# Kernel tuning notes

Measured on AMD Instinct MI355X. Metric: run time of the kernel, lower is better.

Reference implementation:

```python
import jax, jax.numpy as jnp
import numpy as np

T, B, OBS, H, A = 128, 256, 128, 512, 18
LSTM_IN = H + A + 1  # trunk_out + one_hot(a) + r


def setup_inputs() -> dict:
    key = jax.random.key(0)
    ks = jax.random.split(key, 24)

    def rn(k, shape, scale=0.05):
        return jax.random.normal(k, shape, dtype=jnp.float32) * scale

    inp = {
        "o": jax.random.normal(ks[0], (T, B, OBS), dtype=jnp.float32),
        "a": jax.random.randint(ks[1], (T, B), 0, A, dtype=jnp.int32),
        "r": jax.random.normal(ks[2], (T, B), dtype=jnp.float32),
        "done": (jax.random.uniform(ks[3], (T, B)) < 0.05).astype(jnp.float32),
        "h0": jax.random.normal(ks[4], (B, H), dtype=jnp.float32) * 0.1,
        "c0": jax.random.normal(ks[5], (B, H), dtype=jnp.float32) * 0.1,
        # trunk
        "tW0": rn(ks[6], (OBS, H)), "tb0": jnp.zeros((H,), jnp.float32),
        "tW1": rn(ks[7], (H, H)), "tb1": jnp.zeros((H,), jnp.float32),
        # LSTM (PyTorch layout: gates stacked as [i, f, g, o])
        "W_ih": rn(ks[8], (4 * H, LSTM_IN)), "W_hh": rn(ks[9], (4 * H, H)),
        "b_ih": jnp.zeros((4 * H,), jnp.float32), "b_hh": jnp.zeros((4 * H,), jnp.float32),
        # advantage head
        "aW0": rn(ks[10], (H, H)), "ab0": jnp.zeros((H,), jnp.float32),
        "aW1": rn(ks[11], (H, A)), "ab1": jnp.zeros((A,), jnp.float32),
        # value head
        "vW0": rn(ks[12], (H, H)), "vb0": jnp.zeros((H,), jnp.float32),
        "vW1": rn(ks[13], (H, 1)), "vb1": jnp.zeros((1,), jnp.float32),
    }
    return inp


def _forward(o, a, r, done, h0, c0, tW0, tb0, tW1, tb1,
             W_ih, W_hh, b_ih, b_hh, aW0, ab0, aW1, ab1, vW0, vb0, vW1, vb1):
    # shared trunk: two Linear+ReLU layers, vectorized over T*B
    hidden = jax.nn.relu(jnp.einsum('tbi,ih->tbh', o, tW0) + tb0)
    hidden = jax.nn.relu(jnp.einsum('tbi,ih->tbh', hidden, tW1) + tb1)
    a_oh = jax.nn.one_hot(a, A, dtype=jnp.float32)          # [T,B,A]
    x = jnp.concatenate([hidden, r[..., None], a_oh], -1)    # [T,B,LSTM_IN]

    # precompute input projection for all steps (not state-dependent)
    xg = jnp.einsum('tbi,gi->tbg', x, W_ih) + b_ih + b_hh    # [T,B,4H]

    def step(carry, inp):
        h, c = carry
        xg_t, d_t = inp
        keep = (1.0 - d_t)[:, None]                          # per-step done reset
        h, c = h * keep, c * keep
        gates = xg_t + h @ W_hh.T                            # [B,4H]
        i, f, g, og = jnp.split(gates, 4, axis=-1)
        c = jax.nn.sigmoid(f) * c + jax.nn.sigmoid(i) * jnp.tanh(g)
        h = jax.nn.sigmoid(og) * jnp.tanh(c)
        return (h, c), h

    (hT, cT), hs = jax.lax.scan(step, (h0, c0), (xg, done))  # hs: [T,B,H]

    ah = jax.nn.relu(jnp.einsum('tbh,hk->tbk', hs, aW0) + ab0)
    adv = jnp.einsum('tbk,ka->tba', ah, aW1) + ab1            # [T,B,A]
    vh = jax.nn.relu(jnp.einsum('tbh,hk->tbk', hs, vW0) + vb0)
    val = jnp.einsum('tbk,kv->tbv', vh, vW1) + vb1            # [T,B,1]
    q = val + (adv - adv.mean(axis=-1, keepdims=True))
    return q, hT, cT


def reference(o, a, r, done, h0, c0, tW0, tb0, tW1, tb1,
              W_ih, W_hh, b_ih, b_hh, aW0, ab0, aW1, ab1, vW0, vb0, vW1, vb1):
    return _forward(o, a, r, done, h0, c0, tW0, tb0, tW1, tb1,
                    W_ih, W_hh, b_ih, b_hh, aW0, ab0, aW1, ab1, vW0, vb0, vW1, vb1)
```

## Files before the change

### kernel.cpp

```cpp
#include <hip/hip_runtime.h>
#include <cstdint>

typedef unsigned short u16;
typedef unsigned int u32;
typedef unsigned long long u64;
typedef float f32x4 __attribute__((ext_vector_type(4)));
typedef short s16x8 __attribute__((ext_vector_type(8)));

#define DEV static __device__ __forceinline__

#define TT 128
#define BB 256
#define OBSD 128
#define HHD 512
#define AD 18
#define GGD 2048
#define MMD 32768

DEV u16 f2bf(float f) {
  u32 u = __builtin_bit_cast(u32, f);
  u += 0x7fffu + ((u >> 16) & 1u);
  return (u16)(u >> 16);
}
DEV float bf2f(u16 h) { return __builtin_bit_cast(float, ((u32)h) << 16); }

DEV f32x4 mfma16x16x32(s16x8 a, s16x8 b, f32x4 c) {
  asm("v_mfma_f32_16x16x32_bf16 %0, %1, %2, %0" : "+v"(c) : "v"(a), "v"(b));
  return c;
}
DEV void fence_mfma_read(f32x4& x) { asm volatile("s_nop 7" : "+v"(x)); }
DEV void fence_mfma_srcc(f32x4& x) { asm volatile("s_nop 1" : "+v"(x)); }

typedef __attribute__((address_space(3))) char lds_char;
typedef __attribute__((address_space(1))) const char gl_char;
DEV void gload16(const char* g, char* l) {
  __builtin_amdgcn_global_load_lds((const gl_char*)g, (lds_char*)l, 16, 0, 0);
}

DEV float sigm(float x) { return 1.f / (1.f + __expf(-x)); }
DEV float tanh_fast(float x) {
  float t = __expf(-2.f * fabsf(x));
  float r = (1.f - t) / (1.f + t);
  return copysignf(r, x);
}

constexpr size_t OFF_FLAGS = 0;
constexpr size_t OFF_HRING = 524288;
constexpr size_t OFF_TW0T  = 1048576;
constexpr size_t OFF_TW1T  = 1179648;
constexpr size_t OFF_AW0T  = 1703936;
constexpr size_t OFF_VW0T  = 2228224;
constexpr size_t OFF_AW1T  = 2752512;
constexpr size_t OFF_VW1T  = 2770944;
constexpr size_t OFF_WIH   = 2772992;
constexpr size_t OFF_WHH   = 4870144;
constexpr size_t OFF_BSUM  = 6967296;
constexpr size_t OFF_WRC   = 6975488;
constexpr size_t OFF_WEMB  = 6983680;
constexpr size_t OFF_BCAT  = 7131136;
constexpr size_t OFF_OBF   = 8388608;
constexpr size_t OFF_BUF1  = 16777216;
constexpr size_t OFF_BUF2  = 50331648;
constexpr size_t OFF_BUF3  = 83886080;

__global__ __launch_bounds__(256) void prep(
    const float* __restrict__ o, const float* __restrict__ tW0,
    const float* __restrict__ tW1, const float* __restrict__ aW0,
    const float* __restrict__ vW0, const float* __restrict__ aW1,
    const float* __restrict__ vW1, const float* __restrict__ Wih,
    const float* __restrict__ WhhF, const float* __restrict__ bih,
    const float* __restrict__ bhh, const float* __restrict__ h0,
    const float* __restrict__ done, const float* __restrict__ ab0,
    const float* __restrict__ vb0,
    u16* __restrict__ o_bf, u16* __restrict__ tW0T, u16* __restrict__ tW1T,
    u16* __restrict__ aW0T, u16* __restrict__ vW0T, u16* __restrict__ aW1T,
    u16* __restrict__ vW1T, u16* __restrict__ WihB, u16* __restrict__ WhhB,
    float* __restrict__ bsum, float* __restrict__ wrc, float* __restrict__ wemb,
    float* __restrict__ bcat, u16* __restrict__ hring)
{
  const int total = 4178432;
  for (int id = blockIdx.x * 256 + threadIdx.x; id < total; id += gridDim.x * 256) {
    int i = id;
    if (i < 1048576) {
      float4 v = ((const float4*)o)[i];
      u16* dst = o_bf + (size_t)i * 4;
      dst[0] = f2bf(v.x); dst[1] = f2bf(v.y); dst[2] = f2bf(v.z); dst[3] = f2bf(v.w);
      continue;
    }
    i -= 1048576;
    if (i < 65536)  { int n = i >> 7, k = i & 127; tW0T[i] = f2bf(tW0[k * 512 + n]); continue; }
    i -= 65536;
    if (i < 262144) { int n = i >> 9, k = i & 511; tW1T[i] = f2bf(tW1[k * 512 + n]); continue; }
    i -= 262144;
    if (i < 262144) { int n = i >> 9, k = i & 511; aW0T[i] = f2bf(aW0[k * 512 + n]); continue; }
    i -= 262144;
    if (i < 262144) { int n = i >> 9, k = i & 511; vW0T[i] = f2bf(vW0[k * 512 + n]); continue; }
    i -= 262144;
    if (i < 9216)   { int n = i >> 9, k = i & 511; aW1T[i] = f2bf(aW1[k * 18 + n]); continue; }
    i -= 9216;
    if (i < 512)    { vW1T[i] = f2bf(vW1[i]); continue; }
    i -= 512;
    if (i < 1048576){ int g = i >> 9, k = i & 511; WihB[i] = f2bf(Wih[g * 531 + k]); continue; }
    i -= 1048576;
    if (i < 1048576){ WhhB[i] = f2bf(WhhF[i]); continue; }
    i -= 1048576;
    if (i < 2048)   { bsum[i] = bih[i] + bhh[i]; wrc[i] = Wih[i * 531 + 512]; continue; }
    i -= 2048;
    if (i < 36864)  { int j = i >> 11, g = i & 2047; wemb[i] = Wih[g * 531 + 513 + j]; continue; }
    i -= 36864;
    if (i < 1024)   { bcat[i] = (i < 512) ? ab0[i] : vb0[i - 512]; continue; }
    i -= 1024;
    { int b = i >> 9; hring[i] = f2bf(h0[i] * (1.f - done[b])); }
  }
}

template<int MODE>
__global__ __launch_bounds__(256) void gemm_bt(
    const u16* __restrict__ A, const u16* __restrict__ Bt, u16* __restrict__ C,
    int Mdim, int Ndim, int Kdim,
    const float* __restrict__ bias,
    const float* __restrict__ wrc, const float* __restrict__ wemb,
    const float* __restrict__ rin, const int* __restrict__ ain)
{
  __shared__ __align__(16) char smem[32768];
  const int tid = threadIdx.x;
  const int nTn = Ndim >> 7;
  int wg = blockIdx.x;
  {
    const int per = gridDim.x >> 3;
    wg = (wg & 7) * per + (wg >> 3);
  }
  const int tm = wg / nTn, tn = wg % nTn;
  const int wid = tid >> 6, lane = tid & 63;
  const int wr = wid >> 1, wc = wid & 1;
  const int l15 = lane & 15, l4 = lane >> 4;

  f32x4 acc[4][4];
#pragma unroll
  for (int i = 0; i < 4; ++i)
#pragma unroll
    for (int j = 0; j < 4; ++j) acc[i][j] = f32x4{0.f, 0.f, 0.f, 0.f};

  const int srow = lane >> 3;
  const int scolb = ((lane & 7) * 16) ^ (srow << 4);
  const size_t kd2 = (size_t)Kdim * 2;
  const char* Abase = (const char*)(A + (size_t)tm * 128 * Kdim);
  const char* Bbase = (const char*)(Bt + (size_t)tn * 128 * Kdim);
  const char* ga[4]; const char* gb[4]; char* la[4]; char* lb[4];
#pragma unroll
  for (int j = 0; j < 4; ++j) {
    const int row = wid * 32 + j * 8 + srow;
    ga[j] = Abase + (size_t)row * kd2 + scolb;
    gb[j] = Bbase + (size_t)row * kd2 + scolb;
    la[j] = smem + wid * 4096 + j * 1024;
    lb[j] = smem + 16384 + wid * 4096 + j * 1024;
  }

  for (int k0 = 0; k0 < Kdim; k0 += 64) {
    const size_t kb = (size_t)k0 * 2;
#pragma unroll
    for (int j = 0; j < 4; ++j) {
      gload16(ga[j] + kb, la[j]);
      gload16(gb[j] + kb, lb[j]);
    }
    __syncthreads();
#pragma unroll
    for (int kk = 0; kk < 2; ++kk) {
      s16x8 af[4], bfr[4];
#pragma unroll
      for (int i = 0; i < 4; ++i) {
        int ar = wr * 64 + i * 16 + l15;
        af[i] = *(const s16x8*)(smem + ((ar * 128 + kk * 64 + l4 * 16) ^ ((ar & 7) << 4)));
        int br = wc * 64 + i * 16 + l15;
        bfr[i] = *(const s16x8*)(smem + 16384 + ((br * 128 + kk * 64 + l4 * 16) ^ ((br & 7) << 4)));
      }
#pragma unroll
      for (int i = 0; i < 4; ++i)
#pragma unroll
        for (int j = 0; j < 4; ++j)
          acc[i][j] = mfma16x16x32(af[i], bfr[j], acc[i][j]);
    }
    __syncthreads();
  }

#pragma unroll
  for (int i = 0; i < 4; ++i)
#pragma unroll
    for (int j = 0; j < 4; ++j) fence_mfma_read(acc[i][j]);

#pragma unroll
  for (int i = 0; i < 4; ++i) {
    const int rowb = tm * 128 + wr * 64 + i * 16 + l4 * 4;
    float rv[4]; int av[4];
    if (MODE == 1) {
#pragma unroll
      for (int r = 0; r < 4; ++r) { rv[r] = rin[rowb + r]; av[r] = ain[rowb + r]; }
    }
#pragma unroll
    for (int j = 0; j < 4; ++j) {
      const int col = tn * 128 + wc * 64 + j * 16 + l15;
      const float bs = bias[col];
      if (MODE == 0) {
#pragma unroll
        for (int r = 0; r < 4; ++r) {
          float x = acc[i][j][r] + bs;
          x = fmaxf(x, 0.f);
          C[(size_t)(rowb + r) * Ndim + col] = f2bf(x);
        }
      } else {
        const float wcv = wrc[col];
#pragma unroll
        for (int r = 0; r < 4; ++r) {
          float x = acc[i][j][r] + bs + rv[r] * wcv + wemb[av[r] * GGD + col];
          C[(size_t)(rowb + r) * Ndim + col] = f2bf(x);
        }
      }
    }
  }
}

__global__ __launch_bounds__(256) void lstm_seq(
    const u16* __restrict__ xg, const u16* __restrict__ WhhB,
    const float* __restrict__ done, const float* __restrict__ c0,
    u16* __restrict__ hring, u16* __restrict__ hs,
    float* __restrict__ hT, float* __restrict__ cT, u32* __restrict__ flags)
{
  __shared__ __align__(16) char wsm[65536];
  const int tid = threadIdx.x;
  const int bg = blockIdx.x & 3;
  const int ug = blockIdx.x >> 2;
  const int b0 = bg * 64;
  const int u0 = ug * 16;

#pragma unroll
  for (int i = 0; i < 16; ++i) {
    int idx = i * 256 + tid;
    int lr = idx >> 6, c8 = idx & 63;
    int g = lr >> 4, uu = lr & 15;
    uint4 v = *(const uint4*)(WhhB + (size_t)(g * 512 + u0 + uu) * 512 + c8 * 8);
    *(uint4*)(wsm + ((lr * 1024 + c8 * 16) ^ ((lr & 7) << 4))) = v;
  }
  __syncthreads();

  const int wid = tid >> 6, lane = tid & 63;
  const int l15 = lane & 15, l4 = lane >> 4;
  const int mrow = wid * 16 + l4 * 4;
  const int afrow = b0 + wid * 16 + l15;
  const int u = u0 + l15;

  float creg[4], kc[4], kn[4];
#pragma unroll
  for (int r = 0; r < 4; ++r) {
    creg[r] = c0[(size_t)(b0 + mrow + r) * HHD + u];
    kc[r] = 1.f - done[b0 + mrow + r];
    kn[r] = 1.f - done[BB + b0 + mrow + r];
  }

  u16 xpf[16];
#pragma unroll
  for (int g = 0; g < 4; ++g)
#pragma unroll
    for (int r = 0; r < 4; ++r)
      xpf[g * 4 + r] = xg[(size_t)(b0 + mrow + r) * GGD + g * HHD + u];

  for (int t = 0; t < TT; ++t) {
    const u16* hsrc = hring + (size_t)(t & 1) * (BB * HHD);
    u16* hdst = hring + (size_t)((t + 1) & 1) * (BB * HHD);

    f32x4 acc[4];
#pragma unroll
    for (int g = 0; g < 4; ++g)
#pragma unroll
      for (int r = 0; r < 4; ++r)
        acc[g][r] = bf2f(xpf[g * 4 + r]);
#pragma unroll
    for (int g = 0; g < 4; ++g) fence_mfma_srcc(acc[g]);

    u64 aflo[16], afhi[16];
    const u64* hb = (const u64*)(hsrc + (size_t)afrow * HHD);
#pragma unroll
    for (int kk = 0; kk < 16; ++kk) {
      aflo[kk] = __hip_atomic_load(hb + kk * 8 + l4 * 2,
                                   __ATOMIC_RELAXED, __HIP_MEMORY_SCOPE_AGENT);
      afhi[kk] = __hip_atomic_load(hb + kk * 8 + l4 * 2 + 1,
                                   __ATOMIC_RELAXED, __HIP_MEMORY_SCOPE_AGENT);
    }
#pragma unroll
    for (int kk = 0; kk < 16; ++kk) {
      union { u64 q[2]; s16x8 v; } tmp;
      tmp.q[0] = aflo[kk]; tmp.q[1] = afhi[kk];
      s16x8 a = tmp.v;
#pragma unroll
      for (int g = 0; g < 4; ++g) {
        int br = g * 16 + l15;
        s16x8 b = *(const s16x8*)(wsm + ((br * 1024 + kk * 64 + l4 * 16) ^ ((br & 7) << 4)));
        acc[g] = mfma16x16x32(a, b, acc[g]);
      }
    }
#pragma unroll
    for (int g = 0; g < 4; ++g) fence_mfma_read(acc[g]);

    float hv_[4], cv_[4];
#pragma unroll
    for (int r = 0; r < 4; ++r) {
      float iv = sigm(acc[0][r]);
      float fv = sigm(acc[1][r]);
      float gv = tanh_fast(acc[2][r]);
      float ov = sigm(acc[3][r]);
      float c = fv * (creg[r] * kc[r]) + iv * gv;
      float h = ov * tanh_fast(c);
      creg[r] = c; cv_[r] = c; hv_[r] = h;
    }

    if (t < TT - 1) {
      u32 pw[4];
#pragma unroll
      for (int r = 0; r < 4; ++r) {
        u16 ob = f2bf(hv_[r] * kn[r]);
        u16 pb = (u16)__shfl_xor((int)ob, 1, 64);
        pw[r] = ((l15 & 1) == 0) ? ((u32)ob | ((u32)pb << 16))
                                 : ((u32)pb | ((u32)ob << 16));
      }
      {
        const int rb = (l15 & 1) * 2;
        u32* hd32 = (u32*)hdst;
        const int col2 = (u0 + (l15 & ~1)) >> 1;
        __hip_atomic_store(&hd32[(size_t)(b0 + mrow + rb) * 256 + col2], pw[rb],
                           __ATOMIC_RELAXED, __HIP_MEMORY_SCOPE_AGENT);
        __hip_atomic_store(&hd32[(size_t)(b0 + mrow + rb + 1) * 256 + col2], pw[rb + 1],
                           __ATOMIC_RELAXED, __HIP_MEMORY_SCOPE_AGENT);
      }
      __syncthreads();
      if (tid == 0)
        __hip_atomic_store(&flags[(bg * TT + t) * 32 + ug], 1u,
                           __ATOMIC_RELAXED, __HIP_MEMORY_SCOPE_AGENT);
#pragma unroll
      for (int r = 0; r < 4; ++r)
        hs[((size_t)t * BB + b0 + mrow + r) * HHD + u] = f2bf(hv_[r]);
#pragma unroll
      for (int g = 0; g < 4; ++g)
#pragma unroll
        for (int r = 0; r < 4; ++r)
          xpf[g * 4 + r] = xg[((size_t)(t + 1) * BB + b0 + mrow + r) * GGD + g * HHD + u];
#pragma unroll
      for (int r = 0; r < 4; ++r) {
        kc[r] = kn[r];
        kn[r] = (t + 2 < TT) ? (1.f - done[(size_t)(t + 2) * BB + b0 + mrow + r]) : 1.f;
      }
      if (tid < 32) {
        while (__hip_atomic_load(&flags[(bg * TT + t) * 32 + tid],
                                 __ATOMIC_RELAXED, __HIP_MEMORY_SCOPE_AGENT) == 0u)
          __builtin_amdgcn_s_sleep(1);
      }
      __syncthreads();
    } else {
#pragma unroll
      for (int r = 0; r < 4; ++r) {
        hs[((size_t)t * BB + b0 + mrow + r) * HHD + u] = f2bf(hv_[r]);
        hT[(size_t)(b0 + mrow + r) * HHD + u] = hv_[r];
        cT[(size_t)(b0 + mrow + r) * HHD + u] = cv_[r];
      }
    }
  }
}

__global__ __launch_bounds__(256) void head_final(
    const u16* __restrict__ hv, const u16* __restrict__ aW1T,
    const u16* __restrict__ vW1T, const float* __restrict__ ab1,
    const float* __restrict__ vb1, float* __restrict__ q)
{
  __shared__ __align__(16) u16 wa[AD * HHD];
  __shared__ __align__(16) u16 wv[HHD];
  const int tid = threadIdx.x;
  for (int i = tid; i < AD * HHD / 8; i += 256) ((uint4*)wa)[i] = ((const uint4*)aW1T)[i];
  for (int i = tid; i < HHD / 8; i += 256) ((uint4*)wv)[i] = ((const uint4*)vW1T)[i];
  __syncthreads();
  const int wid = tid >> 6, lane = tid & 63;
  for (int row = blockIdx.x * 4 + wid; row < MMD; row += gridDim.x * 4) {
    uint4 va = *(const uint4*)(hv + (size_t)row * 1024 + lane * 8);
    uint4 vv = *(const uint4*)(hv + (size_t)row * 1024 + 512 + lane * 8);
    const u16* pa = (const u16*)&va;
    const u16* pv = (const u16*)&vv;
    float af[8], vf[8];
#pragma unroll
    for (int j = 0; j < 8; ++j) { af[j] = bf2f(pa[j]); vf[j] = bf2f(pv[j]); }
    float accs[19];
#pragma unroll
    for (int n = 0; n < 19; ++n) accs[n] = 0.f;
#pragma unroll
    for (int n = 0; n < AD; ++n) {
      const u16* w = wa + n * HHD + lane * 8;
#pragma unroll
      for (int j = 0; j < 8; ++j) accs[n] += af[j] * bf2f(w[j]);
    }
    {
      const u16* w = wv + lane * 8;
#pragma unroll
      for (int j = 0; j < 8; ++j) accs[18] += vf[j] * bf2f(w[j]);
    }
#pragma unroll
    for (int n = 0; n < 19; ++n) {
#pragma unroll
      for (int off = 32; off > 0; off >>= 1)
        accs[n] += __shfl_xor(accs[n], off, 64);
    }
    if (lane == 0) {
      float s = 0.f;
      float advv[AD];
#pragma unroll
      for (int n = 0; n < AD; ++n) { advv[n] = accs[n] + ab1[n]; s += advv[n]; }
      float val = accs[18] + vb1[0];
      float mean = s * (1.f / 18.f);
#pragma unroll
      for (int n = 0; n < AD; ++n) q[(size_t)row * AD + n] = val + advv[n] - mean;
    }
  }
}

extern "C" void kernel_launch(void* const* d_in, const int* in_sizes, int n_in,
                              void* d_out, int out_size, void* d_ws, size_t ws_size,
                              hipStream_t stream) {
  const float* o    = (const float*)d_in[0];
  const int*   a    = (const int*)d_in[1];
  const float* r    = (const float*)d_in[2];
  const float* done = (const float*)d_in[3];
  const float* h0   = (const float*)d_in[4];
  const float* c0   = (const float*)d_in[5];
  const float* tW0  = (const float*)d_in[6];
  const float* tb0  = (const float*)d_in[7];
  const float* tW1  = (const float*)d_in[8];
  const float* tb1  = (const float*)d_in[9];
  const float* Wih  = (const float*)d_in[10];
  const float* Whh  = (const float*)d_in[11];
  const float* bih  = (const float*)d_in[12];
  const float* bhh  = (const float*)d_in[13];
  const float* aW0  = (const float*)d_in[14];
  const float* ab0  = (const float*)d_in[15];
  const float* aW1  = (const float*)d_in[16];
  const float* ab1  = (const float*)d_in[17];
  const float* vW0  = (const float*)d_in[18];
  const float* vb0  = (const float*)d_in[19];
  const float* vW1  = (const float*)d_in[20];
  const float* vb1  = (const float*)d_in[21];
  (void)in_sizes; (void)n_in; (void)ws_size;

  char* ws = (char*)d_ws;
  u32* flags  = (u32*)(ws + OFF_FLAGS);
  u16* hring  = (u16*)(ws + OFF_HRING);
  u16* tW0T   = (u16*)(ws + OFF_TW0T);
  u16* tW1T   = (u16*)(ws + OFF_TW1T);
  u16* aW0T   = (u16*)(ws + OFF_AW0T);
  u16* vW0T   = (u16*)(ws + OFF_VW0T);
  u16* aW1T   = (u16*)(ws + OFF_AW1T);
  u16* vW1T   = (u16*)(ws + OFF_VW1T);
  u16* WihB   = (u16*)(ws + OFF_WIH);
  u16* WhhB   = (u16*)(ws + OFF_WHH);
  float* bsum = (float*)(ws + OFF_BSUM);
  float* wrc  = (float*)(ws + OFF_WRC);
  float* wemb = (float*)(ws + OFF_WEMB);
  float* bcat = (float*)(ws + OFF_BCAT);
  u16* o_bf   = (u16*)(ws + OFF_OBF);
  u16* buf1   = (u16*)(ws + OFF_BUF1);
  u16* buf2   = (u16*)(ws + OFF_BUF2);
  u16* buf3   = (u16*)(ws + OFF_BUF3);

  float* qout = (float*)d_out;
  float* hT   = qout + (size_t)TT * BB * AD;
  float* cT   = hT + (size_t)BB * HHD;

  hipMemsetAsync(flags, 0, 65536, stream);
  prep<<<2048, 256, 0, stream>>>(o, tW0, tW1, aW0, vW0, aW1, vW1, Wih, Whh,
                                 bih, bhh, h0, done, ab0, vb0,
                                 o_bf, tW0T, tW1T, aW0T, vW0T, aW1T, vW1T,
                                 WihB, WhhB, bsum, wrc, wemb, bcat, hring);
  gemm_bt<0><<<1024, 256, 0, stream>>>(o_bf, tW0T, buf1, MMD, 512, 128, tb0,
                                       nullptr, nullptr, nullptr, nullptr);
  gemm_bt<0><<<1024, 256, 0, stream>>>(buf1, tW1T, buf2, MMD, 512, 512, tb1,
                                       nullptr, nullptr, nullptr, nullptr);
  gemm_bt<1><<<4096, 256, 0, stream>>>(buf2, WihB, buf3, MMD, 2048, 512, bsum,
                                       wrc, wemb, r, a);
  lstm_seq<<<128, 256, 0, stream>>>(buf3, WhhB, done, c0, hring,
                                    buf1 , hT, cT, flags);
  gemm_bt<0><<<2048, 256, 0, stream>>>(buf1 , aW0T, buf3 , MMD, 1024, 512, bcat,
                                       nullptr, nullptr, nullptr, nullptr);
  head_final<<<2048, 256, 0, stream>>>(buf3, aW1T, vW1T, ab1, vb1, qout);
}
```

Measured before the change: 1.112 ms.

## Fuse LSTM input projection into recurrent kernel and use counter barrier

Removes the separate input-projection GEMM and instead computes W_ih·x for step t+1 inside the LSTM kernel, with W_ih tiles held in a second 64KB LDS buffer. This overlaps the work with the inter-block wait and avoids writing and reading the large gate tensor. The per-step barrier now uses one atomic counter per step instead of 32 flags polled by 32 threads. The trade-off is extra MFMA work and LDS pressure in the latency-bound sequential kernel.

```diff
diff --git a/kernel.cpp b/kernel.cpp
--- a/kernel.cpp
+++ b/kernel.cpp
@@ -114,13 +114,9 @@
   }
 }
 
-template<int MODE>
 __global__ __launch_bounds__(256) void gemm_bt(
     const u16* __restrict__ A, const u16* __restrict__ Bt, u16* __restrict__ C,
-    int Mdim, int Ndim, int Kdim,
-    const float* __restrict__ bias,
-    const float* __restrict__ wrc, const float* __restrict__ wemb,
-    const float* __restrict__ rin, const int* __restrict__ ain)
+    int Mdim, int Ndim, int Kdim, const float* __restrict__ bias)
 {
   __shared__ __align__(16) char smem[32768];
   const int tid = threadIdx.x;
@@ -191,41 +187,31 @@
 #pragma unroll
   for (int i = 0; i < 4; ++i) {
     const int rowb = tm * 128 + wr * 64 + i * 16 + l4 * 4;
-    float rv[4]; int av[4];
-    if (MODE == 1) {
-#pragma unroll
-      for (int r = 0; r < 4; ++r) { rv[r] = rin[rowb + r]; av[r] = ain[rowb + r]; }
-    }
 #pragma unroll
     for (int j = 0; j < 4; ++j) {
       const int col = tn * 128 + wc * 64 + j * 16 + l15;
       const float bs = bias[col];
-      if (MODE == 0) {
-#pragma unroll
-        for (int r = 0; r < 4; ++r) {
-          float x = acc[i][j][r] + bs;
-          x = fmaxf(x, 0.f);
-          C[(size_t)(rowb + r) * Ndim + col] = f2bf(x);
-        }
-      } else {
-        const float wcv = wrc[col];
-#pragma unroll
-        for (int r = 0; r < 4; ++r) {
-          float x = acc[i][j][r] + bs + rv[r] * wcv + wemb[av[r] * GGD + col];
-          C[(size_t)(rowb + r) * Ndim + col] = f2bf(x);
-        }
+#pragma unroll
+      for (int r = 0; r < 4; ++r) {
+        float x = acc[i][j][r] + bs;
+        x = fmaxf(x, 0.f);
+        C[(size_t)(rowb + r) * Ndim + col] = f2bf(x);
       }
     }
   }
 }
 
 __global__ __launch_bounds__(256) void lstm_seq(
-    const u16* __restrict__ xg, const u16* __restrict__ WhhB,
-    const float* __restrict__ done, const float* __restrict__ c0,
+    const u16* __restrict__ hid, const u16* __restrict__ WhhB,
+    const u16* __restrict__ WihB, const float* __restrict__ done,
+    const float* __restrict__ c0, const float* __restrict__ rin,
+    const int* __restrict__ ain, const float* __restrict__ bsum,
+    const float* __restrict__ wrc, const float* __restrict__ wemb,
     u16* __restrict__ hring, u16* __restrict__ hs,
-    float* __restrict__ hT, float* __restrict__ cT, u32* __restrict__ flags)
+    float* __restrict__ hT, float* __restrict__ cT, u32* __restrict__ cnt)
 {
   __shared__ __align__(16) char wsm[65536];
+  __shared__ __align__(16) char wsi[65536];
   const int tid = threadIdx.x;
   const int bg = blockIdx.x & 3;
   const int ug = blockIdx.x >> 2;
@@ -237,8 +223,9 @@
     int idx = i * 256 + tid;
     int lr = idx >> 6, c8 = idx & 63;
     int g = lr >> 4, uu = lr & 15;
-    uint4 v = *(const uint4*)(WhhB + (size_t)(g * 512 + u0 + uu) * 512 + c8 * 8);
-    *(uint4*)(wsm + ((lr * 1024 + c8 * 16) ^ ((lr & 7) << 4))) = v;
+    int sb = (lr * 1024 + c8 * 16) ^ ((lr & 7) << 4);
+    *(uint4*)(wsm + sb) = *(const uint4*)(WhhB + (size_t)(g * 512 + u0 + uu) * 512 + c8 * 8);
+    *(uint4*)(wsi + sb) = *(const uint4*)(WihB + (size_t)(g * 512 + u0 + uu) * 512 + c8 * 8);
   }
   __syncthreads();
 
@@ -248,6 +235,10 @@
   const int afrow = b0 + wid * 16 + l15;
   const int u = u0 + l15;
 
+  float bsv[4], wrv[4];
+#pragma unroll
+  for (int g = 0; g < 4; ++g) { bsv[g] = bsum[g * 512 + u]; wrv[g] = wrc[g * 512 + u]; }
+
   float creg[4], kc[4], kn[4];
 #pragma unroll
   for (int r = 0; r < 4; ++r) {
@@ -256,25 +247,37 @@
     kn[r] = 1.f - done[BB + b0 + mrow + r];
   }
 
-  u16 xpf[16];
-#pragma unroll
-  for (int g = 0; g < 4; ++g)
-#pragma unroll
-    for (int r = 0; r < 4; ++r)
-      xpf[g * 4 + r] = xg[(size_t)(b0 + mrow + r) * GGD + g * HHD + u];
+  f32x4 acc[4];
+  {
+    float rv[4]; int av[4];
+#pragma unroll
+    for (int r = 0; r < 4; ++r) { rv[r] = rin[b0 + mrow + r]; av[r] = ain[b0 + mrow + r]; }
+#pragma unroll
+    for (int g = 0; g < 4; ++g)
+#pragma unroll
+      for (int r = 0; r < 4; ++r)
+        acc[g][r] = bsv[g] + rv[r] * wrv[g] + wemb[av[r] * GGD + g * 512 + u];
+#pragma unroll
+    for (int g = 0; g < 4; ++g) fence_mfma_srcc(acc[g]);
+    uint4 hfr[16];
+#pragma unroll
+    for (int kk = 0; kk < 16; ++kk)
+      hfr[kk] = *(const uint4*)(hid + (size_t)afrow * HHD + kk * 32 + l4 * 8);
+#pragma unroll
+    for (int kk = 0; kk < 16; ++kk) {
+      s16x8 a = __builtin_bit_cast(s16x8, hfr[kk]);
+#pragma unroll
+      for (int g = 0; g < 4; ++g) {
+        int br = g * 16 + l15;
+        s16x8 b = *(const s16x8*)(wsi + ((br * 1024 + kk * 64 + l4 * 16) ^ ((br & 7) << 4)));
+        acc[g] = mfma16x16x32(a, b, acc[g]);
+      }
+    }
+  }
 
   for (int t = 0; t < TT; ++t) {
     const u16* hsrc = hring + (size_t)(t & 1) * (BB * HHD);
     u16* hdst = hring + (size_t)((t + 1) & 1) * (BB * HHD);
-
-    f32x4 acc[4];
-#pragma unroll
-    for (int g = 0; g < 4; ++g)
-#pragma unroll
-      for (int r = 0; r < 4; ++r)
-        acc[g][r] = bf2f(xpf[g * 4 + r]);
-#pragma unroll
-    for (int g = 0; g < 4; ++g) fence_mfma_srcc(acc[g]);
 
     u64 aflo[16], afhi[16];
     const u64* hb = (const u64*)(hsrc + (size_t)afrow * HHD);
@@ -332,24 +335,50 @@
       }
       __syncthreads();
       if (tid == 0)
-        __hip_atomic_store(&flags[(bg * TT + t) * 32 + ug], 1u,
-                           __ATOMIC_RELAXED, __HIP_MEMORY_SCOPE_AGENT);
+        __hip_atomic_fetch_add(&cnt[bg * TT + t], 1u,
+                               __ATOMIC_RELAXED, __HIP_MEMORY_SCOPE_AGENT);
+
 #pragma unroll
       for (int r = 0; r < 4; ++r)
         hs[((size_t)t * BB + b0 + mrow + r) * HHD + u] = f2bf(hv_[r]);
+
+      uint4 hfr[16];
+#pragma unroll
+      for (int kk = 0; kk < 16; ++kk)
+        hfr[kk] = *(const uint4*)(hid + ((size_t)(t + 1) * BB + afrow) * HHD + kk * 32 + l4 * 8);
+
+      float rv[4]; int av[4];
+#pragma unroll
+      for (int r = 0; r < 4; ++r) {
+        rv[r] = rin[(size_t)(t + 1) * BB + b0 + mrow + r];
+        av[r] = ain[(size_t)(t + 1) * BB + b0 + mrow + r];
+      }
 #pragma unroll
       for (int g = 0; g < 4; ++g)
 #pragma unroll
         for (int r = 0; r < 4; ++r)
-          xpf[g * 4 + r] = xg[((size_t)(t + 1) * BB + b0 + mrow + r) * GGD + g * HHD + u];
+          acc[g][r] = bsv[g] + rv[r] * wrv[g] + wemb[av[r] * GGD + g * 512 + u];
+#pragma unroll
+      for (int g = 0; g < 4; ++g) fence_mfma_srcc(acc[g]);
+#pragma unroll
+      for (int kk = 0; kk < 16; ++kk) {
+        s16x8 a = __builtin_bit_cast(s16x8, hfr[kk]);
+#pragma unroll
+        for (int g = 0; g < 4; ++g) {
+          int br = g * 16 + l15;
+          s16x8 b = *(const s16x8*)(wsi + ((br * 1024 + kk * 64 + l4 * 16) ^ ((br & 7) << 4)));
+          acc[g] = mfma16x16x32(a, b, acc[g]);
+        }
+      }
 #pragma unroll
       for (int r = 0; r < 4; ++r) {
         kc[r] = kn[r];
         kn[r] = (t + 2 < TT) ? (1.f - done[(size_t)(t + 2) * BB + b0 + mrow + r]) : 1.f;
       }
-      if (tid < 32) {
-        while (__hip_atomic_load(&flags[(bg * TT + t) * 32 + tid],
-                                 __ATOMIC_RELAXED, __HIP_MEMORY_SCOPE_AGENT) == 0u)
+
+      if (tid == 0) {
+        while (__hip_atomic_load(&cnt[bg * TT + t],
+                                 __ATOMIC_RELAXED, __HIP_MEMORY_SCOPE_AGENT) < 32u)
           __builtin_amdgcn_s_sleep(1);
       }
       __syncthreads();
@@ -473,15 +502,10 @@
                                  bih, bhh, h0, done, ab0, vb0,
                                  o_bf, tW0T, tW1T, aW0T, vW0T, aW1T, vW1T,
                                  WihB, WhhB, bsum, wrc, wemb, bcat, hring);
-  gemm_bt<0><<<1024, 256, 0, stream>>>(o_bf, tW0T, buf1, MMD, 512, 128, tb0,
-                                       nullptr, nullptr, nullptr, nullptr);
-  gemm_bt<0><<<1024, 256, 0, stream>>>(buf1, tW1T, buf2, MMD, 512, 512, tb1,
-                                       nullptr, nullptr, nullptr, nullptr);
-  gemm_bt<1><<<4096, 256, 0, stream>>>(buf2, WihB, buf3, MMD, 2048, 512, bsum,
-                                       wrc, wemb, r, a);
-  lstm_seq<<<128, 256, 0, stream>>>(buf3, WhhB, done, c0, hring,
-                                    buf1 , hT, cT, flags);
-  gemm_bt<0><<<2048, 256, 0, stream>>>(buf1 , aW0T, buf3 , MMD, 1024, 512, bcat,
-                                       nullptr, nullptr, nullptr, nullptr);
+  gemm_bt<<<1024, 256, 0, stream>>>(o_bf, tW0T, buf1, MMD, 512, 128, tb0);
+  gemm_bt<<<1024, 256, 0, stream>>>(buf1, tW1T, buf2, MMD, 512, 512, tb1);
+  lstm_seq<<<128, 256, 0, stream>>>(buf2 , WhhB, WihB, done, c0, r, a,
+                                    bsum, wrc, wemb, hring, buf1 , hT, cT, flags);
+  gemm_bt<<<2048, 256, 0, stream>>>(buf1 , aW0T, buf3 , MMD, 1024, 512, bcat);
   head_final<<<2048, 256, 0, stream>>>(buf3, aW1T, vW1T, ab1, vb1, qout);
 }
```

After: 1.423 ms. 1.28x slower.
